# Kernel tuning notes

Measured on AMD Instinct MI355X. Metric: run time of the kernel, lower is better.

The kernel has to match this reference:

```python
import jax, jax.numpy as jnp
import numpy as np

E, D, H, B, S = 16, 1024, 256, 4, 4096  # num_splats, model_dim, ff_dim//num_splats, batch, seq_len


def setup_inputs() -> dict:
    key = jax.random.key(0)
    ks = jax.random.split(key, 8)
    s = 0.02  # init scale for stability
    return {
        "x": jax.random.normal(ks[0], (B, S, D), dtype=jnp.float32),
        "splat_id": jax.random.randint(ks[1], (S,), 0, E, dtype=jnp.int32),
        "W1": jax.random.normal(ks[2], (E, D, H), dtype=jnp.float32) * s,
        "b1": jnp.zeros((E, H), dtype=jnp.float32),
        "W2": jax.random.normal(ks[3], (E, H, D), dtype=jnp.float32) * s,
        "b2": jnp.zeros((E, D), dtype=jnp.float32),
        "Wg1": jax.random.normal(ks[4], (D, D), dtype=jnp.float32) * s,
        "bg1": jnp.zeros((D,), dtype=jnp.float32),
        "Wg2": jax.random.normal(ks[5], (D, D), dtype=jnp.float32) * s,
        "bg2": jnp.zeros((D,), dtype=jnp.float32),
    }


def reference(x, splat_id, W1, b1, W2, b2, Wg1, bg1, Wg2, bg2):
    # Splat-aware dispatch: token s is processed by expert splat_id[s].
    # Equivalent vectorized form: run every expert's small MLP, mask at the
    # hidden layer by expert assignment, and sum over experts (each token is
    # assigned to exactly one expert, matching the gather->MLP->scatter loop).
    nE = W1.shape[0]
    onehot = (splat_id[None, :] == jnp.arange(nE, dtype=splat_id.dtype)[:, None]).astype(x.dtype)  # [E,S]
    # hidden: [E,B,S,H]
    h = jax.nn.gelu(jnp.einsum('bsd,edh->ebsh', x, W1) + b1[:, None, None, :], approximate=False)
    h = h * onehot[:, None, :, None]  # zero tokens not routed to expert e
    routed = jnp.einsum('ebsh,ehd->bsd', h, W2)  # [B,S,D]
    routed = routed + jnp.einsum('es,ed->sd', onehot, b2)[None, :, :]  # per-token expert bias
    # global aggregator MLP (torch GELU default = exact erf form)
    g = jax.nn.gelu(routed @ Wg1 + bg1, approximate=False)
    return g @ Wg2 + bg2
```

## Files before the change

### kernel.cpp

```cpp
#include <hip/hip_runtime.h>


#define DEV __device__ __forceinline__

typedef float f32x4 __attribute__((ext_vector_type(4)));
typedef short short8 __attribute__((ext_vector_type(8)));

DEV unsigned short f2bf(float f) {
  unsigned u = __float_as_uint(f);
  u += 0x7fffu + ((u >> 16) & 1u);
  return (unsigned short)(u >> 16);
}

DEV void gload16(const void* g, void* l) {
  __builtin_amdgcn_global_load_lds(
      (const __attribute__((address_space(1))) unsigned int*)g,
      (__attribute__((address_space(3))) unsigned int*)l, 16, 0, 0);
}

DEV float gelu_exact(float v) {
  return 0.5f * v * (1.0f + erff(v * 0.70710678118654752f));
}

__global__ __launch_bounds__(256) void prep_kernel(
    const float* __restrict__ x, unsigned short* __restrict__ xb,
    const float* __restrict__ W1, unsigned short* __restrict__ w1t,
    const float* __restrict__ W2, unsigned short* __restrict__ w2t,
    const float* __restrict__ Wg1, unsigned short* __restrict__ wg1t,
    const float* __restrict__ Wg2, unsigned short* __restrict__ wg2t) {
  __shared__ float tile[64][65];
  const int t = threadIdx.x;
  int id = (int)blockIdx.x;
  if (id < 8192) {
    long i = ((long)id * 256 + t) * 8;
    float4 v0 = *(const float4*)(x + i);
    float4 v1 = *(const float4*)(x + i + 4);
    uint4 o;
    o.x = (unsigned)f2bf(v0.x) | ((unsigned)f2bf(v0.y) << 16);
    o.y = (unsigned)f2bf(v0.z) | ((unsigned)f2bf(v0.w) << 16);
    o.z = (unsigned)f2bf(v1.x) | ((unsigned)f2bf(v1.y) << 16);
    o.w = (unsigned)f2bf(v1.z) | ((unsigned)f2bf(v1.w) << 16);
    *(uint4*)(xb + i) = o;
    return;
  }
  id -= 8192;
  const float* in; unsigned short* out;
  int R, C, r0, c0; long base;
  if (id < 1024) {
    in = W1; out = w1t; R = 1024; C = 256;
    base = (long)(id >> 6) * 262144;
    r0 = ((id >> 2) & 15) * 64; c0 = (id & 3) * 64;
  } else if (id < 2048) {
    id -= 1024;
    in = W2; out = w2t; R = 256; C = 1024;
    base = (long)(id >> 6) * 262144;
    r0 = ((id >> 4) & 3) * 64; c0 = (id & 15) * 64;
  } else if (id < 2304) {
    id -= 2048;
    in = Wg1; out = wg1t; R = 1024; C = 1024; base = 0;
    r0 = (id >> 4) * 64; c0 = (id & 15) * 64;
  } else {
    id -= 2304;
    in = Wg2; out = wg2t; R = 1024; C = 1024; base = 0;
    r0 = (id >> 4) * 64; c0 = (id & 15) * 64;
  }
  const int cc = t & 63, rr = t >> 6;
#pragma unroll
  for (int i = 0; i < 16; i++) {
    int r = rr + i * 4;
    tile[r][cc] = in[base + (long)(r0 + r) * C + (c0 + cc)];
  }
  __syncthreads();
#pragma unroll
  for (int i = 0; i < 16; i++) {
    int c = rr + i * 4;
    out[base + (long)(c0 + c) * R + (r0 + cc)] = f2bf(tile[cc][c]);
  }
}

__global__ __launch_bounds__(256) void route_kernel(
    const int* __restrict__ sid, int S, int* __restrict__ offs, int* __restrict__ order,
    int* __restrict__ tileE, int* __restrict__ tileR, int* __restrict__ ntl) {
  __shared__ int cnt[16], cur[16];
  const int t = threadIdx.x;
  if (t < 16) cnt[t] = 0;
  __syncthreads();
  for (int s = t; s < S; s += 256) atomicAdd(&cnt[sid[s]], 1);
  __syncthreads();
  if (t == 0) {
    int a = 0;
    for (int e = 0; e < 16; e++) { offs[e] = a; cur[e] = a; a += cnt[e]; }
    offs[16] = a;
    int nt = 0;
    for (int e = 0; e < 16; e++) {
      const int rows = 4 * cnt[e];
      for (int r = 0; r < rows; r += 128) {
        tileE[nt] = e;
        tileR[nt] = 4 * offs[e] + r;
        nt++;
      }
    }
    ntl[0] = nt;
  }
  __syncthreads();
  for (int s = t; s < S; s += 256) {
    int p = atomicAdd(&cur[sid[s]], 1);
    order[p] = s;
  }
}

template <bool GATHER_A, bool SCATTER_C, bool GELU, bool OUT_F32>
__global__ __launch_bounds__(256) void gemm_mfma(
    const unsigned short* __restrict__ A, const unsigned short* __restrict__ BT,
    const float* __restrict__ bias, void* __restrict__ Cout,
    int N, int K,
    const int* __restrict__ order, const int* __restrict__ offs,
    const int* __restrict__ tileE, const int* __restrict__ tileR,
    const int* __restrict__ ntl,
    int S, long btStride, int biasStride) {
  const int ti = (int)blockIdx.y;
  if (ti >= ntl[0]) return;
  const int t = (int)threadIdx.x;
  const int lane = t & 63;
  const int w = t >> 6;
  const int wm = w >> 1, wn = w & 1;
  const int tileN = (int)blockIdx.x;

  const int e = tileE[ti];
  const int rowBase = tileR[ti];
  int Me = 4 * offs[e + 1] - rowBase;
  if (Me > 128) Me = 128;
  const unsigned short* bt = BT + (long)e * btStride;
  const float* bs = bias + (long)e * biasStride;

  __shared__ __align__(16) unsigned short lA[128 * 64];
  __shared__ __align__(16) unsigned short lB[128 * 64];

  const unsigned short* aSrc[4];
  const unsigned short* bSrc[4];
  {
    const int q = t & 7;
#pragma unroll
    for (int i = 0; i < 4; i++) {
      const int row = i * 32 + (t >> 3);
      const int koff = ((q * 16) ^ ((row & 7) << 4)) >> 1;
      const int rr = (row < Me) ? row : (Me - 1);
      const int g = rowBase + rr;
      long arow;
      if (GATHER_A) {
        const int s = order[g >> 2];
        arow = (long)(g & 3) * S + s;
      } else {
        arow = g;
      }
      aSrc[i] = A + arow * (long)K + koff;
      const int col = tileN * 128 + row;
      bSrc[i] = bt + (long)col * K + koff;
    }
  }

  f32x4 acc[4][4] = {};

  const int KT = K >> 6;
  for (int kt = 0; kt < KT; kt++) {
    __syncthreads();
#pragma unroll
    for (int i = 0; i < 4; i++) {
      gload16(aSrc[i] + (kt << 6), (void*)(lA + i * 2048 + w * 512));
      gload16(bSrc[i] + (kt << 6), (void*)(lB + i * 2048 + w * 512));
    }
    __syncthreads();
#pragma unroll
    for (int kk = 0; kk < 2; kk++) {
      short8 af[4], bfr[4];
      const int kbyte = kk * 64 + (lane >> 4) * 16;
#pragma unroll
      for (int mi = 0; mi < 4; mi++) {
        const int row = wm * 64 + mi * 16 + (lane & 15);
        const int off = row * 128 + (kbyte ^ ((row & 7) << 4));
        af[mi] = *(const short8*)((const char*)lA + off);
      }
#pragma unroll
      for (int ni = 0; ni < 4; ni++) {
        const int row = wn * 64 + ni * 16 + (lane & 15);
        const int off = row * 128 + (kbyte ^ ((row & 7) << 4));
        bfr[ni] = *(const short8*)((const char*)lB + off);
      }
#pragma unroll
      for (int mi = 0; mi < 4; mi++)
#pragma unroll
        for (int ni = 0; ni < 4; ni++)
          acc[mi][ni] = __builtin_amdgcn_mfma_f32_16x16x32_bf16(af[mi], bfr[ni], acc[mi][ni], 0, 0, 0);
    }
  }

  float bcol[4];
#pragma unroll
  for (int ni = 0; ni < 4; ni++)
    bcol[ni] = bs[tileN * 128 + wn * 64 + ni * 16 + (lane & 15)];

#pragma unroll
  for (int mi = 0; mi < 4; mi++) {
#pragma unroll
    for (int j = 0; j < 4; j++) {
      const int lrow = wm * 64 + mi * 16 + ((lane >> 4) * 4) + j;
      if (lrow >= Me) continue;
      const int g = rowBase + lrow;
      long crow;
      if (SCATTER_C) crow = (long)(g & 3) * S + order[g >> 2];
      else crow = g;
#pragma unroll
      for (int ni = 0; ni < 4; ni++) {
        float v = acc[mi][ni][j] + bcol[ni];
        if (GELU) v = gelu_exact(v);
        const long cidx = crow * (long)N + tileN * 128 + wn * 64 + ni * 16 + (lane & 15);
        if (OUT_F32) ((float*)Cout)[cidx] = v;
        else ((unsigned short*)Cout)[cidx] = f2bf(v);
      }
    }
  }
}

template <bool GELU, bool OUT_F32>
__global__ __launch_bounds__(256, 4) void gemm_dense128(
    const unsigned short* __restrict__ A, const unsigned short* __restrict__ BT,
    const float* __restrict__ bias, void* __restrict__ Cout,
    int N, int K, int ntiles) {
  const int t = (int)threadIdx.x;
  const int lane = t & 63;
  const int w = t >> 6;
  const int wm = w >> 1, wn = w & 1;

  const int cpx = (int)gridDim.x >> 3;
  const int swz = ((int)blockIdx.x & 7) * cpx + ((int)blockIdx.x >> 3);
  const int mtile = swz / ntiles, ntile = swz % ntiles;

  __shared__ __align__(16) unsigned short lA[128 * 64];
  __shared__ __align__(16) unsigned short lB[128 * 64];

  const unsigned short* aSrc[4];
  const unsigned short* bSrc[4];
  {
    const int q = t & 7;
#pragma unroll
    for (int i = 0; i < 4; i++) {
      const int row = i * 32 + (t >> 3);
      const int koff = ((q * 16) ^ ((row & 7) << 4)) >> 1;
      aSrc[i] = A + (long)(mtile * 128 + row) * K + koff;
      bSrc[i] = BT + (long)(ntile * 128 + row) * K + koff;
    }
  }

  f32x4 acc[4][4] = {};

  const int KT = K >> 6;
  for (int kt = 0; kt < KT; kt++) {
    __syncthreads();
#pragma unroll
    for (int i = 0; i < 4; i++) {
      gload16(aSrc[i] + (kt << 6), (void*)(lA + i * 2048 + w * 512));
      gload16(bSrc[i] + (kt << 6), (void*)(lB + i * 2048 + w * 512));
    }
    __syncthreads();
#pragma unroll
    for (int kk = 0; kk < 2; kk++) {
      short8 af[4], bfr[4];
      const int kbyte = kk * 64 + (lane >> 4) * 16;
#pragma unroll
      for (int mi = 0; mi < 4; mi++) {
        const int row = wm * 64 + mi * 16 + (lane & 15);
        const int off = row * 128 + (kbyte ^ ((row & 7) << 4));
        af[mi] = *(const short8*)((const char*)lA + off);
      }
#pragma unroll
      for (int ni = 0; ni < 4; ni++) {
        const int row = wn * 64 + ni * 16 + (lane & 15);
        const int off = row * 128 + (kbyte ^ ((row & 7) << 4));
        bfr[ni] = *(const short8*)((const char*)lB + off);
      }
#pragma unroll
      for (int mi = 0; mi < 4; mi++)
#pragma unroll
        for (int ni = 0; ni < 4; ni++)
          acc[mi][ni] = __builtin_amdgcn_mfma_f32_16x16x32_bf16(af[mi], bfr[ni], acc[mi][ni], 0, 0, 0);
    }
  }

  float bcol[4];
#pragma unroll
  for (int ni = 0; ni < 4; ni++)
    bcol[ni] = bias[ntile * 128 + wn * 64 + ni * 16 + (lane & 15)];

#pragma unroll
  for (int mi = 0; mi < 4; mi++) {
#pragma unroll
    for (int j = 0; j < 4; j++) {
      const long crow = mtile * 128 + wm * 64 + mi * 16 + ((lane >> 4) * 4) + j;
#pragma unroll
      for (int ni = 0; ni < 4; ni++) {
        float v = acc[mi][ni][j] + bcol[ni];
        if (GELU) v = gelu_exact(v);
        const long cidx = crow * (long)N + ntile * 128 + wn * 64 + ni * 16 + (lane & 15);
        if (OUT_F32) ((float*)Cout)[cidx] = v;
        else ((unsigned short*)Cout)[cidx] = f2bf(v);
      }
    }
  }
}

extern "C" void kernel_launch(void* const* d_in, const int* in_sizes, int n_in,
                              void* d_out, int out_size, void* d_ws, size_t ws_size,
                              hipStream_t stream) {
  const float* x   = (const float*)d_in[0];
  const int*   sid = (const int*)d_in[1];
  const float* W1  = (const float*)d_in[2];
  const float* b1  = (const float*)d_in[3];
  const float* W2  = (const float*)d_in[4];
  const float* b2  = (const float*)d_in[5];
  const float* Wg1 = (const float*)d_in[6];
  const float* bg1 = (const float*)d_in[7];
  const float* Wg2 = (const float*)d_in[8];
  const float* bg2 = (const float*)d_in[9];
  (void)in_sizes; (void)n_in; (void)out_size; (void)ws_size;

  constexpr int D = 1024, H = 256, S = 4096, B = 4;
  constexpr long NT = (long)B * S;

  char* ws = (char*)d_ws;
  unsigned short* xb   = (unsigned short*)(ws);
  unsigned short* w1t  = (unsigned short*)(ws + 33554432);
  unsigned short* w2t  = (unsigned short*)(ws + 41943040);
  unsigned short* wg1t = (unsigned short*)(ws + 50331648);
  unsigned short* wg2t = (unsigned short*)(ws + 52428800);
  unsigned short* hbuf = (unsigned short*)(ws + 54525952);
  unsigned short* rout = (unsigned short*)(ws + 62914560);
  int* offs  = (int*)(ws + 96468992);
  int* order = (int*)(ws + 96469248);
  int* tileE = (int*)(ws + 96485632);
  int* tileR = (int*)(ws + 96486208);
  int* ntl   = (int*)(ws + 96486784);

  prep_kernel<<<dim3(10752), 256, 0, stream>>>(x, xb, W1, w1t, W2, w2t, Wg1, wg1t, Wg2, wg2t);
  route_kernel<<<1, 256, 0, stream>>>(sid, S, offs, order, tileE, tileR, ntl);

  gemm_mfma<true, false, true, false><<<dim3(H / 128, 144), 256, 0, stream>>>(
      xb, w1t, b1, hbuf, H, D, order, offs, tileE, tileR, ntl, S, (long)H * D, H);
  gemm_mfma<false, true, false, false><<<dim3(D / 128, 144), 256, 0, stream>>>(
      hbuf, w2t, b2, rout, D, H, order, offs, tileE, tileR, ntl, S, (long)D * H, D);
  gemm_dense128<true, false><<<dim3((unsigned)(NT / 128) * (D / 128)), 256, 0, stream>>>(
      rout, wg1t, bg1, xb, D, D, D / 128);
  gemm_dense128<false, true><<<dim3((unsigned)(NT / 128) * (D / 128)), 256, 0, stream>>>(
      xb, wg2t, bg2, d_out, D, D, D / 128);
}
```

Measured before the change: 182.8 us.

## Fuse x fp32-to-bf16 conversion into gathered first expert GEMM with 64-row tiles

Removes the separate pass that converts all of x to bf16 in the prep kernel. The first expert GEMM now reads fp32 x rows directly through the routing gather, converts them in registers, and writes them into swizzled LDS, with the next k-step prefetched into registers. It also switches to 64-row tiles (new routing tile lists) to launch more blocks, since N=256 gives few column tiles. This saves a 64MB read plus a 32MB write, but the first GEMM now reads twice as many A bytes and does the conversion work on its critical path.

```diff
diff --git a/kernel.cpp b/kernel.cpp
--- a/kernel.cpp
+++ b/kernel.cpp
@@ -23,7 +23,6 @@
 }
 
 __global__ __launch_bounds__(256) void prep_kernel(
-    const float* __restrict__ x, unsigned short* __restrict__ xb,
     const float* __restrict__ W1, unsigned short* __restrict__ w1t,
     const float* __restrict__ W2, unsigned short* __restrict__ w2t,
     const float* __restrict__ Wg1, unsigned short* __restrict__ wg1t,
@@ -31,19 +30,6 @@
   __shared__ float tile[64][65];
   const int t = threadIdx.x;
   int id = (int)blockIdx.x;
-  if (id < 8192) {
-    long i = ((long)id * 256 + t) * 8;
-    float4 v0 = *(const float4*)(x + i);
-    float4 v1 = *(const float4*)(x + i + 4);
-    uint4 o;
-    o.x = (unsigned)f2bf(v0.x) | ((unsigned)f2bf(v0.y) << 16);
-    o.y = (unsigned)f2bf(v0.z) | ((unsigned)f2bf(v0.w) << 16);
-    o.z = (unsigned)f2bf(v1.x) | ((unsigned)f2bf(v1.y) << 16);
-    o.w = (unsigned)f2bf(v1.z) | ((unsigned)f2bf(v1.w) << 16);
-    *(uint4*)(xb + i) = o;
-    return;
-  }
-  id -= 8192;
   const float* in; unsigned short* out;
   int R, C, r0, c0; long base;
   if (id < 1024) {
@@ -80,7 +66,8 @@
 
 __global__ __launch_bounds__(256) void route_kernel(
     const int* __restrict__ sid, int S, int* __restrict__ offs, int* __restrict__ order,
-    int* __restrict__ tileE, int* __restrict__ tileR, int* __restrict__ ntl) {
+    int* __restrict__ tileE, int* __restrict__ tileR, int* __restrict__ ntl,
+    int* __restrict__ t64E, int* __restrict__ t64R, int* __restrict__ ntl64) {
   __shared__ int cnt[16], cur[16];
   const int t = threadIdx.x;
   if (t < 16) cnt[t] = 0;
@@ -91,16 +78,18 @@
     int a = 0;
     for (int e = 0; e < 16; e++) { offs[e] = a; cur[e] = a; a += cnt[e]; }
     offs[16] = a;
-    int nt = 0;
+    int nt = 0, n64 = 0;
     for (int e = 0; e < 16; e++) {
       const int rows = 4 * cnt[e];
       for (int r = 0; r < rows; r += 128) {
-        tileE[nt] = e;
-        tileR[nt] = 4 * offs[e] + r;
-        nt++;
+        tileE[nt] = e; tileR[nt] = 4 * offs[e] + r; nt++;
+      }
+      for (int r = 0; r < rows; r += 64) {
+        t64E[n64] = e; t64R[n64] = 4 * offs[e] + r; n64++;
       }
     }
     ntl[0] = nt;
+    ntl64[0] = n64;
   }
   __syncthreads();
   for (int s = t; s < S; s += 256) {
@@ -109,10 +98,123 @@
   }
 }
 
-template <bool GATHER_A, bool SCATTER_C, bool GELU, bool OUT_F32>
-__global__ __launch_bounds__(256) void gemm_mfma(
+__global__ __launch_bounds__(256, 4) void gemm_g1(
+    const float* __restrict__ x,
+    const unsigned short* __restrict__ w1t, const float* __restrict__ b1,
+    unsigned short* __restrict__ hbuf,
+    const int* __restrict__ order, const int* __restrict__ offs,
+    const int* __restrict__ t64E, const int* __restrict__ t64R,
+    const int* __restrict__ ntl64) {
+  constexpr int S = 4096, D = 1024, H = 256;
+  const int ti = (int)blockIdx.y;
+  if (ti >= ntl64[0]) return;
+  const int ntile = (int)blockIdx.x;
+  const int t = (int)threadIdx.x;
+  const int lane = t & 63;
+  const int wn = t >> 6;
+
+  const int e = t64E[ti];
+  const int rowBase = t64R[ti];
+  int Me = 4 * offs[e + 1] - rowBase;
+  if (Me > 64) Me = 64;
+
+  __shared__ __align__(16) unsigned short lA[64 * 64];
+  __shared__ __align__(16) unsigned short lB[128 * 64];
+
+  const float* xsrc[2];
+  int aDst[2];
+#pragma unroll
+  for (int i = 0; i < 2; i++) {
+    const int row = i * 32 + (t >> 3);
+    const int koff = (((t & 7) * 16) ^ ((row & 7) << 4)) >> 1;
+    const int rr = (row < Me) ? row : (Me - 1);
+    const int g = rowBase + rr;
+    xsrc[i] = x + ((long)(g & 3) * S + order[g >> 2]) * D + koff;
+    aDst[i] = row * 64 + (t & 7) * 8;
+  }
+  const unsigned short* bSrc[4];
+#pragma unroll
+  for (int i = 0; i < 4; i++) {
+    const int row = i * 32 + (t >> 3);
+    bSrc[i] = w1t + (long)e * H * D + (long)(ntile * 128 + row) * D +
+              ((((t & 7) * 16) ^ ((row & 7) << 4)) >> 1);
+  }
+  const int dstE = (t >> 3) * 64 + (t & 7) * 8;
+
+  f32x4 acc[4][2] = {};
+  float4 xv[2][2];
+#pragma unroll
+  for (int i = 0; i < 2; i++) {
+    xv[i][0] = *(const float4*)(xsrc[i]);
+    xv[i][1] = *(const float4*)(xsrc[i] + 4);
+  }
+
+  for (int kt = 0; kt < 16; kt++) {
+    __syncthreads();
+#pragma unroll
+    for (int i = 0; i < 2; i++) {
+      short8 av;
+      av[0] = (short)f2bf(xv[i][0].x); av[1] = (short)f2bf(xv[i][0].y);
+      av[2] = (short)f2bf(xv[i][0].z); av[3] = (short)f2bf(xv[i][0].w);
+      av[4] = (short)f2bf(xv[i][1].x); av[5] = (short)f2bf(xv[i][1].y);
+      av[6] = (short)f2bf(xv[i][1].z); av[7] = (short)f2bf(xv[i][1].w);
+      *(short8*)(lA + aDst[i]) = av;
+    }
+#pragma unroll
+    for (int i = 0; i < 4; i++)
+      gload16(bSrc[i] + (kt << 6), lB + i * 2048 + dstE);
+    if (kt < 15) {
+#pragma unroll
+      for (int i = 0; i < 2; i++) {
+        xv[i][0] = *(const float4*)(xsrc[i] + (kt + 1) * 64);
+        xv[i][1] = *(const float4*)(xsrc[i] + (kt + 1) * 64 + 4);
+      }
+    }
+    __syncthreads();
+#pragma unroll
+    for (int kk = 0; kk < 2; kk++) {
+      short8 aF[4], bF[2];
+      const int kb = kk * 64 + ((lane >> 4) << 4);
+#pragma unroll
+      for (int mi = 0; mi < 4; mi++) {
+        const int row = mi * 16 + (lane & 15);
+        aF[mi] = *(const short8*)((const char*)lA + row * 128 + (kb ^ ((row & 7) << 4)));
+      }
+#pragma unroll
+      for (int ni = 0; ni < 2; ni++) {
+        const int row = wn * 32 + ni * 16 + (lane & 15);
+        bF[ni] = *(const short8*)((const char*)lB + row * 128 + (kb ^ ((row & 7) << 4)));
+      }
+#pragma unroll
+      for (int mi = 0; mi < 4; mi++)
+#pragma unroll
+        for (int ni = 0; ni < 2; ni++)
+          acc[mi][ni] = __builtin_amdgcn_mfma_f32_16x16x32_bf16(aF[mi], bF[ni], acc[mi][ni], 0, 0, 0);
+    }
+  }
+
+  float bc[2];
+#pragma unroll
+  for (int ni = 0; ni < 2; ni++)
+    bc[ni] = b1[e * H + ntile * 128 + wn * 32 + ni * 16 + (lane & 15)];
+#pragma unroll
+  for (int mi = 0; mi < 4; mi++)
+#pragma unroll
+    for (int j = 0; j < 4; j++) {
+      const int lrow = mi * 16 + ((lane >> 4) << 2) + j;
+      if (lrow >= Me) continue;
+      const long crow = rowBase + lrow;
+#pragma unroll
+      for (int ni = 0; ni < 2; ni++) {
+        const float v = gelu_exact(acc[mi][ni][j] + bc[ni]);
+        hbuf[crow * H + ntile * 128 + wn * 32 + ni * 16 + (lane & 15)] = f2bf(v);
+      }
+    }
+}
+
+__global__ __launch_bounds__(256) void gemm_g2(
     const unsigned short* __restrict__ A, const unsigned short* __restrict__ BT,
-    const float* __restrict__ bias, void* __restrict__ Cout,
+    const float* __restrict__ bias, unsigned short* __restrict__ Cout,
     int N, int K,
     const int* __restrict__ order, const int* __restrict__ offs,
     const int* __restrict__ tileE, const int* __restrict__ tileR,
@@ -146,14 +248,7 @@
       const int koff = ((q * 16) ^ ((row & 7) << 4)) >> 1;
       const int rr = (row < Me) ? row : (Me - 1);
       const int g = rowBase + rr;
-      long arow;
-      if (GATHER_A) {
-        const int s = order[g >> 2];
-        arow = (long)(g & 3) * S + s;
-      } else {
-        arow = g;
-      }
-      aSrc[i] = A + arow * (long)K + koff;
+      aSrc[i] = A + (long)g * K + koff;
       const int col = tileN * 128 + row;
       bSrc[i] = bt + (long)col * K + koff;
     }
@@ -206,16 +301,11 @@
       const int lrow = wm * 64 + mi * 16 + ((lane >> 4) * 4) + j;
       if (lrow >= Me) continue;
       const int g = rowBase + lrow;
-      long crow;
-      if (SCATTER_C) crow = (long)(g & 3) * S + order[g >> 2];
-      else crow = g;
+      const long crow = (long)(g & 3) * S + order[g >> 2];
 #pragma unroll
       for (int ni = 0; ni < 4; ni++) {
-        float v = acc[mi][ni][j] + bcol[ni];
-        if (GELU) v = gelu_exact(v);
-        const long cidx = crow * (long)N + tileN * 128 + wn * 64 + ni * 16 + (lane & 15);
-        if (OUT_F32) ((float*)Cout)[cidx] = v;
-        else ((unsigned short*)Cout)[cidx] = f2bf(v);
+        const float v = acc[mi][ni][j] + bcol[ni];
+        Cout[crow * (long)N + tileN * 128 + wn * 64 + ni * 16 + (lane & 15)] = f2bf(v);
       }
     }
   }
@@ -327,7 +417,7 @@
   constexpr long NT = (long)B * S;
 
   char* ws = (char*)d_ws;
-  unsigned short* xb   = (unsigned short*)(ws);
+  unsigned short* gbuf = (unsigned short*)(ws);
   unsigned short* w1t  = (unsigned short*)(ws + 33554432);
   unsigned short* w2t  = (unsigned short*)(ws + 41943040);
   unsigned short* wg1t = (unsigned short*)(ws + 50331648);
@@ -339,16 +429,19 @@
   int* tileE = (int*)(ws + 96485632);
   int* tileR = (int*)(ws + 96486208);
   int* ntl   = (int*)(ws + 96486784);
-
-  prep_kernel<<<dim3(10752), 256, 0, stream>>>(x, xb, W1, w1t, W2, w2t, Wg1, wg1t, Wg2, wg2t);
-  route_kernel<<<1, 256, 0, stream>>>(sid, S, offs, order, tileE, tileR, ntl);
-
-  gemm_mfma<true, false, true, false><<<dim3(H / 128, 144), 256, 0, stream>>>(
-      xb, w1t, b1, hbuf, H, D, order, offs, tileE, tileR, ntl, S, (long)H * D, H);
-  gemm_mfma<false, true, false, false><<<dim3(D / 128, 144), 256, 0, stream>>>(
+  int* t64E  = (int*)(ws + 96487424);
+  int* t64R  = (int*)(ws + 96488704);
+  int* ntl64 = (int*)(ws + 96489984);
+
+  prep_kernel<<<dim3(2560), 256, 0, stream>>>(W1, w1t, W2, w2t, Wg1, wg1t, Wg2, wg2t);
+  route_kernel<<<1, 256, 0, stream>>>(sid, S, offs, order, tileE, tileR, ntl, t64E, t64R, ntl64);
+
+  gemm_g1<<<dim3(H / 128, 272), 256, 0, stream>>>(
+      x, w1t, b1, hbuf, order, offs, t64E, t64R, ntl64);
+  gemm_g2<<<dim3(D / 128, 144), 256, 0, stream>>>(
       hbuf, w2t, b2, rout, D, H, order, offs, tileE, tileR, ntl, S, (long)D * H, D);
   gemm_dense128<true, false><<<dim3((unsigned)(NT / 128) * (D / 128)), 256, 0, stream>>>(
-      rout, wg1t, bg1, xb, D, D, D / 128);
+      rout, wg1t, bg1, gbuf, D, D, D / 128);
   gemm_dense128<false, true><<<dim3((unsigned)(NT / 128) * (D / 128)), 256, 0, stream>>>(
-      xb, wg2t, bg2, d_out, D, D, D / 128);
-}
+      gbuf, wg2t, bg2, d_out, D, D, D / 128);
+}
```

New measurement: 181.3 us. No clear change (-0.8%).
